# Optimization experiments

Hardware: AMD Instinct MI355X
Metric: run time of the kernel (lower is better)

Reference implementation:

```python
import jax, jax.numpy as jnp
from jax import lax
import numpy as np

NBASE = 4
INSIZE = 256
SIZE = NBASE * (2 + 2 * NBASE)  # 40
NTIME, NBATCH = 2000, 128


def crfrle_log_partition(weights, nbase):
    # weights: (ntime, nbatch, 2*nbase*nbase)
    ntime, nbatch, nstate = weights.shape
    eye = jnp.eye(nbase, dtype=weights.dtype)
    ee = jnp.concatenate([eye, eye], axis=1)          # (nbase, 2*nbase)
    holes = -1e30 * ee                                # mask diagonal out for move
    diag = -1e30 * (1.0 - ee)                         # keep only diagonal for stay

    def step(fwd, w_t):
        # fwd: (nbatch, 2*nbase); w_t: (nbatch, 2*nbase*nbase)
        w_mat = w_t.reshape(nbatch, nbase, 2 * nbase)
        ft = fwd[:, None, :]                          # (nbatch, 1, 2*nbase)
        move = jax.scipy.special.logsumexp(ft + w_mat + holes, axis=2)
        stay = jax.scipy.special.logsumexp(ft + w_mat + diag, axis=2)
        return jnp.concatenate([move, stay], axis=1), None

    fwd0 = jnp.zeros((nbatch, 2 * nbase), dtype=weights.dtype)
    fwd, _ = lax.scan(step, fwd0, weights)
    return jax.scipy.special.logsumexp(fwd, axis=1, keepdims=True)  # (nbatch, 1)


def setup_inputs() -> dict:
    key = jax.random.key(0)
    kx, kw, kb = jax.random.split(key, 3)
    x = jax.random.normal(kx, (NTIME, NBATCH, INSIZE), dtype=jnp.float32)
    sd = 0.5 / np.sqrt(INSIZE + SIZE)
    W = sd * jax.random.truncated_normal(kw, -2.0, 2.0, (SIZE, INSIZE), dtype=jnp.float32)
    b = 0.5 * jax.random.truncated_normal(kb, -2.0, 2.0, (SIZE,), dtype=jnp.float32)
    return {"x": x, "W": W, "b": b}


def reference(x, W, b):
    ntime = x.shape[0]
    y = jnp.einsum('tbi,oi->tbo', x, W) + b           # (ntime, nbatch, SIZE)
    shape_p = 1.0 + jax.nn.softplus(y[..., :NBASE])
    scale_p = 0.1 + jax.nn.softplus(y[..., NBASE:2 * NBASE])
    trans = 5.0 * jnp.tanh(y[..., 2 * NBASE:])        # (ntime, nbatch, 2*nbase^2)
    logZ = crfrle_log_partition(trans, NBASE)[None] / ntime  # (1, nbatch, 1)
    return jnp.concatenate([shape_p, scale_p, trans - logZ], axis=2)
```

## Files before the change

### kernel.cpp

```cpp
#include <hip/hip_runtime.h>
#include <hip/hip_bf16.h>

#define NTIME   2000
#define NBATCH  128
#define INSIZE  256
#define NOUT    40
#define NROWS   (NTIME * NBATCH)
#define CCHUNK  80
#define LSTEP   25

typedef __attribute__((ext_vector_type(8))) short  short8;
typedef __attribute__((ext_vector_type(4))) float  float4v;

#define L2E 1.4426950408889634f
#define LN2 0.6931471805599453f

__device__ __forceinline__ float fexp2(float x){ return __builtin_amdgcn_exp2f(x); }
__device__ __forceinline__ float flog2(float x){ return __builtin_amdgcn_logf(x);  }

__device__ __forceinline__ short f2bf(float f) {
    unsigned u = __float_as_uint(f);
    unsigned r = u + 0x7fffu + ((u >> 16) & 1u);
    return (short)(r >> 16);
}

__global__ __launch_bounds__(256) void gemm_act(const float* __restrict__ x,
                                                const float* __restrict__ W,
                                                const float* __restrict__ bias,
                                                float* __restrict__ out)
{
    const int tid  = threadIdx.x;
    const int wave = tid >> 6, lane = tid & 63;
    const int l16  = lane & 15, quad = lane >> 4;
    const long rowBase = (long)blockIdx.x * 128 + wave * 32;

    float4v acc[2][3];
#pragma unroll
    for (int mi = 0; mi < 2; ++mi)
#pragma unroll
        for (int ni = 0; ni < 3; ++ni)
            acc[mi][ni] = (float4v){0.f, 0.f, 0.f, 0.f};

    const float* xp0 = x + (rowBase + l16) * (long)INSIZE + quad * 8;
    const float* xp1 = xp0 + 16 * INSIZE;

    const float* wrow[3];
    float        wmsk[3];
#pragma unroll
    for (int ni = 0; ni < 3; ++ni) {
        int row = ni * 16 + l16;
        wrow[ni] = W + (long)(row < NOUT ? row : 0) * INSIZE + quad * 8;
        wmsk[ni] = (row < NOUT) ? 1.f : 0.f;
    }

#pragma unroll
    for (int s = 0; s < 8; ++s) {
        short8 afrag[2];
#pragma unroll
        for (int mi = 0; mi < 2; ++mi) {
            const float* xp = (mi ? xp1 : xp0) + s * 32;
            float4v xa = *(const float4v*)xp;
            float4v xb = *(const float4v*)(xp + 4);
            short8 a;
            a[0] = f2bf(xa[0]); a[1] = f2bf(xa[1]); a[2] = f2bf(xa[2]); a[3] = f2bf(xa[3]);
            a[4] = f2bf(xb[0]); a[5] = f2bf(xb[1]); a[6] = f2bf(xb[2]); a[7] = f2bf(xb[3]);
            afrag[mi] = a;
        }
#pragma unroll
        for (int ni = 0; ni < 3; ++ni) {
            const float* wp = wrow[ni] + s * 32;
            float m = wmsk[ni];
            float4v wa = *(const float4v*)wp;
            float4v wb = *(const float4v*)(wp + 4);
            short8 bfrag;
            bfrag[0] = f2bf(wa[0] * m); bfrag[1] = f2bf(wa[1] * m);
            bfrag[2] = f2bf(wa[2] * m); bfrag[3] = f2bf(wa[3] * m);
            bfrag[4] = f2bf(wb[0] * m); bfrag[5] = f2bf(wb[1] * m);
            bfrag[6] = f2bf(wb[2] * m); bfrag[7] = f2bf(wb[3] * m);
            acc[0][ni] = __builtin_amdgcn_mfma_f32_16x16x32_bf16(afrag[0], bfrag, acc[0][ni], 0, 0, 0);
            acc[1][ni] = __builtin_amdgcn_mfma_f32_16x16x32_bf16(afrag[1], bfrag, acc[1][ni], 0, 0, 0);
        }
    }

#pragma unroll
    for (int mi = 0; mi < 2; ++mi) {
        long row0 = rowBase + mi * 16 + quad * 4;
#pragma unroll
        for (int ni = 0; ni < 3; ++ni) {
            int o = ni * 16 + l16;
            if (o >= NOUT) continue;
            float bv = bias[o];
#pragma unroll
            for (int r = 0; r < 4; ++r) {
                float y = acc[mi][ni][r] + bv;
                float val;
                if (o < 8) {
                    float sp = fmaxf(y, 0.f) + LN2 * flog2(1.f + fexp2(-fabsf(y) * L2E));
                    val = (o < 4 ? 1.0f : 0.1f) + sp;
                } else {
                    float e = fexp2(2.f * fabsf(y) * L2E);
                    float t = 1.f - 2.f / (e + 1.f);
                    val = 5.f * copysignf(t, y);
                }
                out[(row0 + r) * NOUT + o] = val;
            }
        }
    }
}

__device__ __forceinline__ void scan_step(float (&m)[8], float4v (&w)[8], const float* reload)
{
    const float* wv = (const float*)&w[0];
    float sa[4][8];
#pragma unroll
    for (int i = 0; i < 4; ++i)
#pragma unroll
        for (int k = 0; k < 8; ++k) sa[i][k] = fmaf(wv[i * 8 + k], L2E, m[k]);
#pragma unroll
    for (int q = 0; q < 8; ++q) w[q] = *(const float4v*)(reload + q * 4);

    float nm[8];
#pragma unroll
    for (int i = 0; i < 4; ++i) {
        float* s = sa[i];
        float a = s[i], b2 = s[i + 4];
        float mx2 = fmaxf(a, b2), mn2 = fminf(a, b2);
        nm[4 + i] = mx2 + flog2(1.f + fexp2(mn2 - mx2));
        s[i] = -1e30f; s[i + 4] = -1e30f;
        float mx = fmaxf(fmaxf(fmaxf(s[0], s[1]), fmaxf(s[2], s[3])),
                         fmaxf(fmaxf(s[4], s[5]), fmaxf(s[6], s[7])));
        float sum = ((fexp2(s[0] - mx) + fexp2(s[1] - mx)) + (fexp2(s[2] - mx) + fexp2(s[3] - mx)))
                  + ((fexp2(s[4] - mx) + fexp2(s[5] - mx)) + (fexp2(s[6] - mx) + fexp2(s[7] - mx)));
        nm[i] = mx + flog2(sum);
    }
#pragma unroll
    for (int i = 0; i < 8; ++i) m[i] = nm[i];
}

__global__ __launch_bounds__(256) void scan_chunks(const float* __restrict__ out,
                                                   float* __restrict__ chunkM)
{
    const int tid   = threadIdx.x;
    const int g     = tid >> 3, j0 = tid & 7;
    const int c     = blockIdx.x >> 2;
    const int batch = ((blockIdx.x & 3) << 5) + g;
    const int t0    = c * LSTEP;

    float m[8];
#pragma unroll
    for (int i = 0; i < 8; ++i) m[i] = (i == j0) ? 0.f : -1e30f;

    const size_t R = (size_t)NBATCH * NOUT;
    const float* base = out + ((size_t)(t0 * NBATCH + batch) * NOUT + 8);

    float4v wA[8], wB[8];
#pragma unroll
    for (int q = 0; q < 8; ++q) wA[q] = *(const float4v*)(base + q * 4);
#pragma unroll
    for (int q = 0; q < 8; ++q) wB[q] = *(const float4v*)(base + R + q * 4);

    for (int it = 0; it < (LSTEP - 1) / 2; ++it) {
        scan_step(m, wA, base + (size_t)(2 * it + 2) * R);
        const float* pB = (2 * it + 3 < LSTEP) ? base + (size_t)(2 * it + 3) * R
                                               : base;
        scan_step(m, wB, pB);
    }
    scan_step(m, wA, base);

    float* dst = chunkM + (((size_t)batch * CCHUNK + c) * 8 + j0) * 8;
#pragma unroll
    for (int i = 0; i < 8; ++i) dst[i] = m[i];
}

#define COMB1(P, CN)                                                                         \
    {                                                                                        \
        float s_[8];                                                                         \
        _Pragma("unroll") for (int j = 0; j < 8; ++j) s_[j] = P[j] + v[j];                   \
        int cl_ = ((CN) < CCHUNK) ? (CN) : (CCHUNK - 1);                                     \
        const float* Mp_ = Mb + (size_t)cl_ * 64 + ip;                                       \
        _Pragma("unroll") for (int j = 0; j < 8; ++j) P[j] = Mp_[j * 8];                     \
        float mx_ = fmaxf(fmaxf(fmaxf(s_[0], s_[1]), fmaxf(s_[2], s_[3])),                   \
                          fmaxf(fmaxf(s_[4], s_[5]), fmaxf(s_[6], s_[7])));                  \
        float sum_ = ((fexp2(s_[0] - mx_) + fexp2(s_[1] - mx_)) +                            \
                      (fexp2(s_[2] - mx_) + fexp2(s_[3] - mx_)))                             \
                   + ((fexp2(s_[4] - mx_) + fexp2(s_[5] - mx_)) +                            \
                      (fexp2(s_[6] - mx_) + fexp2(s_[7] - mx_)));                            \
        float nv_ = mx_ + flog2(sum_);                                                       \
        _Pragma("unroll") for (int j = 0; j < 8; ++j) v[j] = __shfl(nv_, gbase + j, 64);     \
    }

__global__ __launch_bounds__(256) void combine_k(const float* __restrict__ chunkM,
                                                 float* __restrict__ logZdiv)
{
    const int tid   = blockIdx.x * 256 + threadIdx.x;
    const int ip    = tid & 7;
    const int batch = tid >> 3;
    const int gbase = (threadIdx.x & 63) & ~7;

    const float* Mb = chunkM + ((size_t)batch * CCHUNK) * 64;

    float v[8];
#pragma unroll
    for (int j = 0; j < 8; ++j) v[j] = 0.f;

    float P0[8], P1[8], P2[8], P3[8];
#pragma unroll
    for (int j = 0; j < 8; ++j) P0[j] = Mb[0 * 64 + j * 8 + ip];
#pragma unroll
    for (int j = 0; j < 8; ++j) P1[j] = Mb[1 * 64 + j * 8 + ip];
#pragma unroll
    for (int j = 0; j < 8; ++j) P2[j] = Mb[2 * 64 + j * 8 + ip];
#pragma unroll
    for (int j = 0; j < 8; ++j) P3[j] = Mb[3 * 64 + j * 8 + ip];

    for (int c = 0; c < CCHUNK; c += 4) {
        COMB1(P0, c + 4)
        COMB1(P1, c + 5)
        COMB1(P2, c + 6)
        COMB1(P3, c + 7)
    }

    float mx = fmaxf(fmaxf(fmaxf(v[0], v[1]), fmaxf(v[2], v[3])),
                     fmaxf(fmaxf(v[4], v[5]), fmaxf(v[6], v[7])));
    float sum = ((fexp2(v[0] - mx) + fexp2(v[1] - mx)) + (fexp2(v[2] - mx) + fexp2(v[3] - mx)))
              + ((fexp2(v[4] - mx) + fexp2(v[5] - mx)) + (fexp2(v[6] - mx) + fexp2(v[7] - mx)));
    float r = mx + flog2(sum);
    if (ip == 0) logZdiv[batch] = r * LN2 / (float)NTIME;
}

__global__ __launch_bounds__(256) void sub_logz(float* __restrict__ out,
                                                const float* __restrict__ logZdiv)
{
    size_t idx = (size_t)blockIdx.x * 256 + threadIdx.x;
    size_t row = idx >> 3;
    int q = (int)(idx & 7);
    int batch = (int)(row & 127);
    float lz = logZdiv[batch];
    float4v* pp = (float4v*)(out + row * NOUT + 8 + q * 4);
    float4v vv = *pp;
    vv[0] -= lz; vv[1] -= lz; vv[2] -= lz; vv[3] -= lz;
    *pp = vv;
}

extern "C" void kernel_launch(void* const* d_in, const int* in_sizes, int n_in,
                              void* d_out, int out_size, void* d_ws, size_t ws_size,
                              hipStream_t stream)
{
    const float* x = (const float*)d_in[0];
    const float* W = (const float*)d_in[1];
    const float* b = (const float*)d_in[2];
    float* out = (float*)d_out;

    char* ws = (char*)d_ws;
    float* chunkM  = (float*)ws;
    float* logZdiv = (float*)(ws + (size_t)NBATCH * CCHUNK * 64 * 4);

    hipLaunchKernelGGL(gemm_act,    dim3(NROWS/128), dim3(256), 0, stream, x, W, b, out);
    hipLaunchKernelGGL(scan_chunks, dim3(CCHUNK*4),  dim3(256), 0, stream, out, chunkM);
    hipLaunchKernelGGL(combine_k,   dim3(4),         dim3(256), 0, stream, chunkM, logZdiv);
    hipLaunchKernelGGL(sub_logz,    dim3(8000),      dim3(256), 0, stream, out, logZdiv);
}
```

Baseline: 426.0 us.

## Fuse scan, combine and logZ subtraction into one persistent kernel with grid barriers

Merges the chunk scan, chunk combine and logZ subtraction kernels into a single persistent 512-block kernel that separates the phases with atomic-counter grid barriers. The barrier counters are reset inside the GEMM kernel. The aim is to remove two kernel-launch gaps and the tail drain between small kernels. The cost is that the subtraction pass runs grid-stride over only 512 blocks, and correctness depends on all 512 blocks being resident at once to avoid deadlock. The combine phase still uses only 4 blocks while the others spin.

```diff
diff --git a/kernel.cpp b/kernel.cpp
--- a/kernel.cpp
+++ b/kernel.cpp
@@ -8,6 +8,7 @@
 #define NROWS   (NTIME * NBATCH)
 #define CCHUNK  80
 #define LSTEP   25
+#define TAILBLK 512
 
 typedef __attribute__((ext_vector_type(8))) short  short8;
 typedef __attribute__((ext_vector_type(4))) float  float4v;
@@ -24,12 +25,25 @@
     return (short)(r >> 16);
 }
 
+__device__ __forceinline__ void grid_bar(unsigned* cnt, unsigned target) {
+    __syncthreads();
+    if (threadIdx.x == 0) {
+        __hip_atomic_fetch_add(cnt, 1u, __ATOMIC_ACQ_REL, __HIP_MEMORY_SCOPE_AGENT);
+        while (__hip_atomic_load(cnt, __ATOMIC_ACQUIRE, __HIP_MEMORY_SCOPE_AGENT) < target)
+            __builtin_amdgcn_s_sleep(2);
+    }
+    __syncthreads();
+}
+
 __global__ __launch_bounds__(256) void gemm_act(const float* __restrict__ x,
                                                 const float* __restrict__ W,
                                                 const float* __restrict__ bias,
-                                                float* __restrict__ out)
+                                                float* __restrict__ out,
+                                                unsigned* __restrict__ bar)
 {
     const int tid  = threadIdx.x;
+    if (blockIdx.x == 0 && tid == 0) { bar[0] = 0u; bar[1] = 0u; }
+
     const int wave = tid >> 6, lane = tid & 63;
     const int l16  = lane & 15, quad = lane >> 4;
     const long rowBase = (long)blockIdx.x * 128 + wave * 32;
@@ -135,41 +149,6 @@
     }
 #pragma unroll
     for (int i = 0; i < 8; ++i) m[i] = nm[i];
-}
-
-__global__ __launch_bounds__(256) void scan_chunks(const float* __restrict__ out,
-                                                   float* __restrict__ chunkM)
-{
-    const int tid   = threadIdx.x;
-    const int g     = tid >> 3, j0 = tid & 7;
-    const int c     = blockIdx.x >> 2;
-    const int batch = ((blockIdx.x & 3) << 5) + g;
-    const int t0    = c * LSTEP;
-
-    float m[8];
-#pragma unroll
-    for (int i = 0; i < 8; ++i) m[i] = (i == j0) ? 0.f : -1e30f;
-
-    const size_t R = (size_t)NBATCH * NOUT;
-    const float* base = out + ((size_t)(t0 * NBATCH + batch) * NOUT + 8);
-
-    float4v wA[8], wB[8];
-#pragma unroll
-    for (int q = 0; q < 8; ++q) wA[q] = *(const float4v*)(base + q * 4);
-#pragma unroll
-    for (int q = 0; q < 8; ++q) wB[q] = *(const float4v*)(base + R + q * 4);
-
-    for (int it = 0; it < (LSTEP - 1) / 2; ++it) {
-        scan_step(m, wA, base + (size_t)(2 * it + 2) * R);
-        const float* pB = (2 * it + 3 < LSTEP) ? base + (size_t)(2 * it + 3) * R
-                                               : base;
-        scan_step(m, wB, pB);
-    }
-    scan_step(m, wA, base);
-
-    float* dst = chunkM + (((size_t)batch * CCHUNK + c) * 8 + j0) * 8;
-#pragma unroll
-    for (int i = 0; i < 8; ++i) dst[i] = m[i];
 }
 
 #define COMB1(P, CN)                                                                         \
@@ -189,57 +168,107 @@
         _Pragma("unroll") for (int j = 0; j < 8; ++j) v[j] = __shfl(nv_, gbase + j, 64);     \
     }
 
-__global__ __launch_bounds__(256) void combine_k(const float* __restrict__ chunkM,
-                                                 float* __restrict__ logZdiv)
-{
-    const int tid   = blockIdx.x * 256 + threadIdx.x;
-    const int ip    = tid & 7;
-    const int batch = tid >> 3;
-    const int gbase = (threadIdx.x & 63) & ~7;
-
-    const float* Mb = chunkM + ((size_t)batch * CCHUNK) * 64;
-
-    float v[8];
-#pragma unroll
-    for (int j = 0; j < 8; ++j) v[j] = 0.f;
-
-    float P0[8], P1[8], P2[8], P3[8];
-#pragma unroll
-    for (int j = 0; j < 8; ++j) P0[j] = Mb[0 * 64 + j * 8 + ip];
-#pragma unroll
-    for (int j = 0; j < 8; ++j) P1[j] = Mb[1 * 64 + j * 8 + ip];
-#pragma unroll
-    for (int j = 0; j < 8; ++j) P2[j] = Mb[2 * 64 + j * 8 + ip];
-#pragma unroll
-    for (int j = 0; j < 8; ++j) P3[j] = Mb[3 * 64 + j * 8 + ip];
-
-    for (int c = 0; c < CCHUNK; c += 4) {
-        COMB1(P0, c + 4)
-        COMB1(P1, c + 5)
-        COMB1(P2, c + 6)
-        COMB1(P3, c + 7)
-    }
-
-    float mx = fmaxf(fmaxf(fmaxf(v[0], v[1]), fmaxf(v[2], v[3])),
-                     fmaxf(fmaxf(v[4], v[5]), fmaxf(v[6], v[7])));
-    float sum = ((fexp2(v[0] - mx) + fexp2(v[1] - mx)) + (fexp2(v[2] - mx) + fexp2(v[3] - mx)))
-              + ((fexp2(v[4] - mx) + fexp2(v[5] - mx)) + (fexp2(v[6] - mx) + fexp2(v[7] - mx)));
-    float r = mx + flog2(sum);
-    if (ip == 0) logZdiv[batch] = r * LN2 / (float)NTIME;
-}
-
-__global__ __launch_bounds__(256) void sub_logz(float* __restrict__ out,
-                                                const float* __restrict__ logZdiv)
-{
-    size_t idx = (size_t)blockIdx.x * 256 + threadIdx.x;
-    size_t row = idx >> 3;
-    int q = (int)(idx & 7);
-    int batch = (int)(row & 127);
-    float lz = logZdiv[batch];
-    float4v* pp = (float4v*)(out + row * NOUT + 8 + q * 4);
-    float4v vv = *pp;
-    vv[0] -= lz; vv[1] -= lz; vv[2] -= lz; vv[3] -= lz;
-    *pp = vv;
+__global__ __launch_bounds__(256, 2) void tail_k(float* __restrict__ out,
+                                                 float* __restrict__ chunkM,
+                                                 float* __restrict__ logZdiv,
+                                                 unsigned* __restrict__ bar)
+{
+    const int tid = threadIdx.x;
+
+    {
+        const int gg = blockIdx.x * 32 + (tid >> 3);
+        if (gg < NBATCH * CCHUNK / 4 * 4 / 4 * 4 && gg < 10240) {
+            const int j0    = tid & 7;
+            const int v_    = gg >> 5;
+            const int gl    = gg & 31;
+            const int c     = v_ >> 2;
+            const int batch = ((v_ & 3) << 5) + gl;
+            const int t0    = c * LSTEP;
+
+            float m[8];
+#pragma unroll
+            for (int i = 0; i < 8; ++i) m[i] = (i == j0) ? 0.f : -1e30f;
+
+            const size_t R = (size_t)NBATCH * NOUT;
+            const float* base = out + ((size_t)(t0 * NBATCH + batch) * NOUT + 8);
+
+            float4v wA[8], wB[8];
+#pragma unroll
+            for (int q = 0; q < 8; ++q) wA[q] = *(const float4v*)(base + q * 4);
+#pragma unroll
+            for (int q = 0; q < 8; ++q) wB[q] = *(const float4v*)(base + R + q * 4);
+
+            for (int it = 0; it < (LSTEP - 1) / 2; ++it) {
+                scan_step(m, wA, base + (size_t)(2 * it + 2) * R);
+                const float* pB = (2 * it + 3 < LSTEP) ? base + (size_t)(2 * it + 3) * R
+                                                       : base;
+                scan_step(m, wB, pB);
+            }
+            scan_step(m, wA, base);
+
+            float* dst = chunkM + (((size_t)batch * CCHUNK + c) * 8 + j0) * 8;
+#pragma unroll
+            for (int i = 0; i < 8; ++i) dst[i] = m[i];
+        }
+    }
+
+    grid_bar(&bar[0], TAILBLK);
+
+    {
+        const int gtid = blockIdx.x * 256 + tid;
+        if (gtid < NBATCH * 8) {
+            const int ip    = gtid & 7;
+            const int batch = gtid >> 3;
+            const int gbase = (tid & 63) & ~7;
+
+            const float* Mb = chunkM + ((size_t)batch * CCHUNK) * 64;
+
+            float v[8];
+#pragma unroll
+            for (int j = 0; j < 8; ++j) v[j] = 0.f;
+
+            float P0[8], P1[8], P2[8], P3[8];
+#pragma unroll
+            for (int j = 0; j < 8; ++j) P0[j] = Mb[0 * 64 + j * 8 + ip];
+#pragma unroll
+            for (int j = 0; j < 8; ++j) P1[j] = Mb[1 * 64 + j * 8 + ip];
+#pragma unroll
+            for (int j = 0; j < 8; ++j) P2[j] = Mb[2 * 64 + j * 8 + ip];
+#pragma unroll
+            for (int j = 0; j < 8; ++j) P3[j] = Mb[3 * 64 + j * 8 + ip];
+
+            for (int c = 0; c < CCHUNK; c += 4) {
+                COMB1(P0, c + 4)
+                COMB1(P1, c + 5)
+                COMB1(P2, c + 6)
+                COMB1(P3, c + 7)
+            }
+
+            float mx = fmaxf(fmaxf(fmaxf(v[0], v[1]), fmaxf(v[2], v[3])),
+                             fmaxf(fmaxf(v[4], v[5]), fmaxf(v[6], v[7])));
+            float sum = ((fexp2(v[0] - mx) + fexp2(v[1] - mx)) + (fexp2(v[2] - mx) + fexp2(v[3] - mx)))
+                      + ((fexp2(v[4] - mx) + fexp2(v[5] - mx)) + (fexp2(v[6] - mx) + fexp2(v[7] - mx)));
+            float r = mx + flog2(sum);
+            if (ip == 0) logZdiv[batch] = r * LN2 / (float)NTIME;
+        }
+    }
+
+    grid_bar(&bar[1], TAILBLK);
+
+    {
+        const size_t nvec   = (size_t)NTIME * NBATCH * 8;
+        const size_t stride = (size_t)TAILBLK * 256;
+        for (size_t idx = (size_t)blockIdx.x * 256 + tid; idx < nvec; idx += stride) {
+            size_t row = idx >> 3;
+            int q = (int)(idx & 7);
+            int batch = (int)(row & 127);
+            float lz = logZdiv[batch];
+            float4v* pp = (float4v*)(out + row * NOUT + 8 + q * 4);
+            float4v vv = *pp;
+            vv[0] -= lz; vv[1] -= lz; vv[2] -= lz; vv[3] -= lz;
+            *pp = vv;
+        }
+    }
 }
 
 extern "C" void kernel_launch(void* const* d_in, const int* in_sizes, int n_in,
@@ -252,11 +281,10 @@
     float* out = (float*)d_out;
 
     char* ws = (char*)d_ws;
-    float* chunkM  = (float*)ws;
-    float* logZdiv = (float*)(ws + (size_t)NBATCH * CCHUNK * 64 * 4);
-
-    hipLaunchKernelGGL(gemm_act,    dim3(NROWS/128), dim3(256), 0, stream, x, W, b, out);
-    hipLaunchKernelGGL(scan_chunks, dim3(CCHUNK*4),  dim3(256), 0, stream, out, chunkM);
-    hipLaunchKernelGGL(combine_k,   dim3(4),         dim3(256), 0, stream, chunkM, logZdiv);
-    hipLaunchKernelGGL(sub_logz,    dim3(8000),      dim3(256), 0, stream, out, logZdiv);
-}
+    float*    chunkM  = (float*)ws;
+    float*    logZdiv = (float*)(ws + 2621440);
+    unsigned* bar     = (unsigned*)(ws + 2621952);
+
+    hipLaunchKernelGGL(gemm_act, dim3(NROWS/128), dim3(256), 0, stream, x, W, b, out, bar);
+    hipLaunchKernelGGL(tail_k,   dim3(TAILBLK),   dim3(256), 0, stream, out, chunkM, logZdiv, bar);
+}
```

New measurement: 568.3 us. 1.33x slower.
